# Kernel optimization log

Measured on AMD Instinct MI355X. Metric: run time of the kernel, lower is better.

Reference implementation:

```python
import jax, jax.numpy as jnp
import numpy as np

V, E, H, M = 32000, 512, 1024, 256
B, T, STRIDE = 2, 2048, 4


def setup_inputs() -> dict:
    key = jax.random.key(0)
    ks = jax.random.split(key, 18)
    s = 0.02
    n = jax.random.normal
    return {
        'input_ids': jax.random.randint(ks[0], (B, T), 0, V),
        'emb_weight': n(ks[1], (V, E)) * s,
        'gru_w_ih': n(ks[2], (3 * H, E)) * s,
        'gru_w_hh': n(ks[3], (3 * H, H)) * s,
        'gru_b_ih': n(ks[4], (3 * H,)) * s,
        'gru_b_hh': n(ks[5], (3 * H,)) * s,
        'q_w': n(ks[6], (M, H)) * s, 'q_b': n(ks[7], (M,)) * s,
        'k_w': n(ks[8], (M, H)) * s, 'k_b': n(ks[9], (M,)) * s,
        'hfc_w': n(ks[10], (4 * E, H)) * s, 'hfc_b': n(ks[11], (4 * E,)) * s,
        'hproj_w': n(ks[12], (E, 4 * E)) * s, 'hproj_b': n(ks[13], (E,)) * s,
        'v_w': n(ks[14], (E, E)) * s,
        'gate_w': n(ks[15], (E, H)) * s, 'gate_b': n(ks[16], (E,)) * s,
        'out_bias': jnp.zeros((V,), jnp.float32),
    }


def _gru(x, w_ih, w_hh, b_ih, b_hh):
    # x: [B,T,E] -> states [B,T,H]; single-layer torch GRU, h0 = 0
    h_dim = w_hh.shape[1]
    xg = jnp.einsum('bte,ge->btg', x, w_ih) + b_ih  # [B,T,3H] input gates precomputed

    def step(h, xg_t):
        gi_r, gi_z, gi_n = jnp.split(xg_t, 3, axis=-1)
        gh = h @ w_hh.T + b_hh
        gh_r, gh_z, gh_n = jnp.split(gh, 3, axis=-1)
        r = jax.nn.sigmoid(gi_r + gh_r)
        z = jax.nn.sigmoid(gi_z + gh_z)
        nstate = jnp.tanh(gi_n + r * gh_n)
        h_new = (1.0 - z) * nstate + z * h
        return h_new, h_new

    h0 = jnp.zeros((x.shape[0], h_dim), x.dtype)
    _, hs = jax.lax.scan(step, h0, jnp.swapaxes(xg, 0, 1))
    return jnp.swapaxes(hs, 0, 1)


def reference(input_ids, emb_weight, gru_w_ih, gru_w_hh, gru_b_ih, gru_b_hh,
              q_w, q_b, k_w, k_b, hfc_w, hfc_b, hproj_w, hproj_b,
              v_w, gate_w, gate_b, out_bias):
    emb = emb_weight[input_ids]                              # [B,T,E]
    states = _gru(emb, gru_w_ih, gru_w_hh, gru_b_ih, gru_b_hh)  # [B,T,H]; dropout is identity in eval

    head = jnp.square(jax.nn.relu(states @ hfc_w.T + hfc_b))  # [B,T,4E]
    base = head @ hproj_w.T + hproj_b                          # [B,T,E]

    # stride source pooling
    src_states = states[:, ::STRIDE]                         # [B,S,H]
    src_values = emb[:, ::STRIDE]                            # [B,S,E]
    seq_len = states.shape[1]
    src_pos = jnp.arange(0, seq_len, STRIDE)                 # [S]
    tgt_pos = jnp.arange(seq_len)                            # [T]
    mask = src_pos[None, :] < tgt_pos[:, None]               # [T,S] causal

    qk = states @ q_w.T + q_b                                # [B,T,M]
    mk = src_states @ k_w.T + k_b                            # [B,S,M]
    scores = jnp.einsum('btm,bsm->bts', qk, mk) / jnp.sqrt(jnp.array(M, qk.dtype))
    neg = jnp.finfo(scores.dtype).min
    scores = jnp.where(mask[None], scores, neg)
    att = jax.nn.softmax(scores, axis=-1)
    att = att * mask[None]
    att = att / jnp.maximum(att.sum(axis=-1, keepdims=True), 1e-6)

    retrieved = jnp.einsum('bts,bse->bte', att, src_values @ v_w.T)  # [B,T,E]
    mixed = base + jax.nn.sigmoid(states @ gate_w.T + gate_b) * retrieved
    return mixed @ emb_weight.T + out_bias                   # [B,T,V] tied logits
```

## Files before the change

### kernel.cpp

```cpp
#include <hip/hip_runtime.h>
#include <stdint.h>

typedef unsigned short u16;
typedef unsigned int u32;
typedef unsigned long long u64;
using f32x4 = __attribute__((ext_vector_type(4))) float;
using s16x8 = __attribute__((ext_vector_type(8))) short;
using s16x4 = __attribute__((ext_vector_type(4))) short;

#define DI __device__ __forceinline__

constexpr int kV = 32000, kE = 512, kH = 1024, kM = 256;
constexpr int kB = 2, kT = 2048, kS = 512;

DI u16 f2bf(float f) {
  u32 u = __float_as_uint(f);
  u32 r = (u + 0x7FFFu + ((u >> 16) & 1u)) >> 16;
  return (u16)r;
}
DI float bf2f(u16 u) { return __uint_as_float(((u32)u) << 16); }

DI void gload_lds16(const void* g, void* l) {
  __builtin_amdgcn_global_load_lds((const __attribute__((address_space(1))) void*)g,
                                   (__attribute__((address_space(3))) void*)l, 16, 0, 0);
}

__global__ __launch_bounds__(256)
void k_cvt(const float* __restrict__ in, u16* __restrict__ out, int n) {
  const int step = gridDim.x * blockDim.x;
  for (int i = blockIdx.x * blockDim.x + threadIdx.x; i * 4 < n; i += step) {
    f32x4 v = *(const f32x4*)(in + (size_t)i * 4);
    ushort4 o;
    o.x = f2bf(v[0]); o.y = f2bf(v[1]); o.z = f2bf(v[2]); o.w = f2bf(v[3]);
    *(ushort4*)(out + (size_t)i * 4) = o;
  }
}

__global__ __launch_bounds__(128)
void k_embed(const int* __restrict__ ids, const float* __restrict__ W,
             u16* __restrict__ out) {
  const int tok = blockIdx.x;
  const int id = ids[tok];
  f32x4 v = ((const f32x4*)(W + (size_t)id * kE))[threadIdx.x];
  ushort4 o;
  o.x = f2bf(v[0]); o.y = f2bf(v[1]); o.z = f2bf(v[2]); o.w = f2bf(v[3]);
  ((ushort4*)(out + (size_t)tok * kE))[threadIdx.x] = o;
}

__global__ __launch_bounds__(256)
void k_stride_copy(const u16* __restrict__ in, u16* __restrict__ out, int rowlen) {
  const int row = blockIdx.x;
  const int b = row / kS, s = row - b * kS;
  const u16* src = in + ((size_t)b * kT + 4 * s) * rowlen;
  u16* dst = out + (size_t)row * rowlen;
  for (int i = threadIdx.x; i < rowlen / 2; i += blockDim.x)
    reinterpret_cast<u32*>(dst)[i] = reinterpret_cast<const u32*>(src)[i];
}

template<int EPI>
__global__ __launch_bounds__(256)
void k_gemm(const u16* __restrict__ A, const u16* __restrict__ Bm,
            float* __restrict__ Cf, u16* __restrict__ Cb,
            const float* __restrict__ bias,
            int Mdim, int Ndim, int Kdim,
            long long sA, long long sB, long long sC,
            const float* __restrict__ addf, const float* __restrict__ mulf) {
  __shared__ __align__(16) u16 lA[128 * 32];
  __shared__ __align__(16) u16 lB[128 * 32];
  const int tid = threadIdx.x;
  const int bz = blockIdx.z;
  A += (long long)bz * sA;
  Bm += (long long)bz * sB;
  const long long coff = (long long)bz * sC;
  const int m0 = blockIdx.y * 128;
  const int n0 = blockIdx.x * 128;
  const int lane = tid & 63;
  const int wm = ((tid >> 6) >> 1) * 64;
  const int wn = ((tid >> 6) & 1) * 64;
  const int sr = tid >> 2;
  const int sc = (tid & 3) * 8;
  f32x4 acc[4][4] = {};
  for (int kt = 0; kt < Kdim; kt += 32) {
    gload_lds16(A + (long long)(m0 + sr) * Kdim + kt + sc,       &lA[tid * 8]);
    gload_lds16(A + (long long)(m0 + 64 + sr) * Kdim + kt + sc,  &lA[(tid + 256) * 8]);
    gload_lds16(Bm + (long long)(n0 + sr) * Kdim + kt + sc,      &lB[tid * 8]);
    gload_lds16(Bm + (long long)(n0 + 64 + sr) * Kdim + kt + sc, &lB[(tid + 256) * 8]);
    __syncthreads();
    s16x8 af[4], bfv[4];
    const int fro = lane & 15;
    const int fk = (lane >> 4) * 8;
#pragma unroll
    for (int f = 0; f < 4; f++) {
      af[f]  = *reinterpret_cast<const s16x8*>(&lA[(wm + f * 16 + fro) * 32 + fk]);
      bfv[f] = *reinterpret_cast<const s16x8*>(&lB[(wn + f * 16 + fro) * 32 + fk]);
    }
#pragma unroll
    for (int i = 0; i < 4; i++)
#pragma unroll
      for (int j = 0; j < 4; j++)
        acc[i][j] = __builtin_amdgcn_mfma_f32_16x16x32_bf16(af[i], bfv[j], acc[i][j], 0, 0, 0);
    __syncthreads();
  }
  const int crow = (lane >> 4) * 4;
  const int ccol = lane & 15;
#pragma unroll
  for (int i = 0; i < 4; i++) {
#pragma unroll
    for (int j = 0; j < 4; j++) {
      const int gn = n0 + wn + j * 16 + ccol;
      const float bs = bias ? bias[gn] : 0.0f;
#pragma unroll
      for (int r = 0; r < 4; r++) {
        const int gm = m0 + wm + i * 16 + crow + r;
        const long long off = coff + (long long)gm * Ndim + gn;
        float v = acc[i][j][r] + bs;
        if constexpr (EPI == 0) {
          Cf[off] = v;
        } else if constexpr (EPI == 1) {
          Cb[off] = f2bf(v);
        } else if constexpr (EPI == 2) {
          float uu = fmaxf(v, 0.0f);
          Cb[off] = f2bf(uu * uu);
        } else {
          float g = 1.0f / (1.0f + __expf(-v));
          Cb[off] = f2bf(addf[off] + g * mulf[off]);
        }
      }
    }
  }
}

__global__ __launch_bounds__(512, 1)
void k_gru(const float* __restrict__ xg, const u16* __restrict__ whh,
           const float* __restrict__ bhh, u64* __restrict__ hbuf,
           u32* __restrict__ flags, u16* __restrict__ states) {
  __shared__ __align__(16) u16 lw[48 * 1024];
  __shared__ __align__(16) float lh[1024];
  __shared__ u32 s_ticket, s_dec, s_res, s_bail;
  const int tid = threadIdx.x;
  u32 xcc;
  asm("s_getreg_b32 %0, hwreg(HW_REG_XCC_ID)" : "=s"(xcc));
  xcc &= 7u;
  if (tid == 0) {
    s_bail = 0u;
    u32 tk = atomicAdd(&flags[128 + xcc], 1u);
    if (tk == 31u) {
      u32 fidx = atomicAdd(&flags[136], 1u);
      if (fidx < 2u)
        __hip_atomic_store(&flags[140 + fidx], xcc + 1u, __ATOMIC_RELAXED, __HIP_MEMORY_SCOPE_AGENT);
    }
    s_ticket = tk;
    u32 d = 0;
    if (blockIdx.x == 0) {
      u32 polls = 0;
      for (;;) {
        if (__hip_atomic_load(&flags[136], __ATOMIC_RELAXED, __HIP_MEMORY_SCOPE_AGENT) >= 2u) {
          u32 a = __hip_atomic_load(&flags[140], __ATOMIC_RELAXED, __HIP_MEMORY_SCOPE_AGENT);
          u32 b = __hip_atomic_load(&flags[141], __ATOMIC_RELAXED, __HIP_MEMORY_SCOPE_AGENT);
          if (a && b) { d = 1u | ((a - 1u) << 8) | ((b - 1u) << 16); break; }
        }
        __builtin_amdgcn_s_sleep(1);
        if (++polls > 500000u) { d = 2u; break; }
      }
      __hip_atomic_store(&flags[137], d, __ATOMIC_RELAXED, __HIP_MEMORY_SCOPE_AGENT);
    } else {
      u32 polls = 0;
      while (!(d = __hip_atomic_load(&flags[137], __ATOMIC_RELAXED, __HIP_MEMORY_SCOPE_AGENT))) {
        __builtin_amdgcn_s_sleep(1);
        if (++polls > 1000000u) { d = 2u; break; }
      }
    }
    s_dec = d;
  }
  __syncthreads();
  const u32 dec = s_dec, ticket = s_ticket;
  int batch = -1;
  u32 slice = 0;
  bool l2m = false;
  if ((dec & 0xFFu) == 1u) {
    const u32 d0 = (dec >> 8) & 0xFFu, d1 = (dec >> 16) & 0xFFu;
    if (xcc == d0 && ticket < 32u) { batch = 0; slice = ticket; l2m = true; }
    else if (xcc == d1 && ticket < 32u) { batch = 1; slice = ticket; l2m = true; }
  } else {
    if (blockIdx.x < 64u) { batch = (int)(blockIdx.x >> 5); slice = blockIdx.x & 31u; }
  }
  if (batch < 0) return;

  if (l2m) {
    u32* hel = &flags[160 + batch * 32];
    u32* vot = &flags[224 + batch * 32];
    if (tid == 0) {
      u32 one = 1u;
      asm volatile("global_store_dword %0, %1, off" :: "v"(&hel[slice]), "v"(one) : "memory");
    }
    bool ok = true;
    if (tid < 32) {
      u32 v = 0, polls = 0;
      const u32* hp = &hel[tid];
      do {
        asm volatile("global_load_dword %0, %1, off nt\n\ts_waitcnt vmcnt(0)"
                     : "=v"(v) : "v"(hp) : "memory");
        if (v) break;
      } while (++polls < 200000u);
      ok = (v != 0);
    }
    u64 bad = __ballot(tid < 32 && !ok);
    if (tid == 0)
      __hip_atomic_store(&vot[slice], bad ? 2u : 1u, __ATOMIC_RELAXED, __HIP_MEMORY_SCOPE_AGENT);
    bool vb = false;
    if (tid < 32) {
      u32 v = 0, polls = 0;
      while (!(v = __hip_atomic_load(&vot[tid], __ATOMIC_RELAXED, __HIP_MEMORY_SCOPE_AGENT)))
        if (++polls > 1000000u) break;
      vb = (v != 1u);
    }
    u64 anybad = __ballot(tid < 32 && vb);
    if (tid == 0) s_res = (anybad == 0ull) ? 1u : 0u;
    __syncthreads();
    if (s_res == 0u) l2m = false;
  }

  const int j0 = (int)slice * 32;
  const int grp = tid >> 4;
  const int gl = tid & 15;
  const int j = j0 + grp;
  s16x4 wreg[3][16];
#pragma unroll
  for (int half = 0; half < 2; half++) {
#pragma unroll
    for (int r = 0; r < 12; r++) {
      int fi = tid + 512 * r;
      int lr = fi >> 7;
      int ce = (fi & 127) * 8;
      int lrow = half * 48 + lr;
      int gate = lrow >> 5, row = lrow & 31;
      gload_lds16(whh + ((size_t)gate * kH + j0 + row) * kH + ce, &lw[fi * 8]);
    }
    __syncthreads();
#pragma unroll
    for (int g = 0; g < 3; g++) {
      const int lrow = g * 32 + grp;
      if (lrow >= half * 48 && lrow < half * 48 + 48) {
        const u16* src = &lw[(size_t)(lrow - half * 48) * 1024];
#pragma unroll
        for (int i = 0; i < 16; i++)
          wreg[g][i] = *(const s16x4*)&src[4 * (gl + 16 * i)];
      }
    }
    __syncthreads();
  }

  const float bhr = bhh[j], bhz = bhh[kH + j], bhn = bhh[2 * kH + j];
  u32* fl = flags + batch * 64;
  const float* xgb = xg + (size_t)batch * kT * 3 * kH;
  u16* stb = states + (size_t)batch * kT * kH;
  float hkeep = 0.0f;
  float gi_r = 0.0f, gi_z = 0.0f, gi_n = 0.0f;
  if (gl == 0) { gi_r = xgb[j]; gi_z = xgb[kH + j]; gi_n = xgb[2 * kH + j]; }
  bool bailed = false;

  for (int t = 0; t < kT; t++) {
    u64* hc = hbuf + (size_t)(t & 1) * (kB * kH) + (size_t)batch * kH;
    u64* hn = hbuf + (size_t)((t + 1) & 1) * (kB * kH) + (size_t)batch * kH;
    const u32 want = (u32)t;
    if (!bailed) {
      u64 v0 = 0, v1 = 0;
      u32 polls = 0;
      if (l2m) {
        const u64* p0 = hc + tid;
        const u64* p1 = hc + tid + 512;
        for (;;) {
          asm volatile(
              "global_load_dwordx2 %0, %2, off nt\n\t"
              "global_load_dwordx2 %1, %3, off nt\n\t"
              "s_waitcnt vmcnt(0)"
              : "=&v"(v0), "=&v"(v1) : "v"(p0), "v"(p1) : "memory");
          if ((u32)(v0 >> 32) >= want && (u32)(v1 >> 32) >= want) break;
          if (++polls > 400000u) { bailed = true; break; }
        }
      } else {
        for (;;) {
          v0 = __hip_atomic_load(hc + tid, __ATOMIC_RELAXED, __HIP_MEMORY_SCOPE_AGENT);
          v1 = __hip_atomic_load(hc + tid + 512, __ATOMIC_RELAXED, __HIP_MEMORY_SCOPE_AGENT);
          if ((u32)(v0 >> 32) >= want && (u32)(v1 >> 32) >= want) break;
          if (++polls > 400000u) { bailed = true; break; }
        }
      }
      lh[tid] = __uint_as_float((u32)v0);
      lh[tid + 512] = __uint_as_float((u32)v1);
    }
    if (bailed) s_bail = 1u;
    __syncthreads();
    bailed = (s_bail != 0u);
    if (tid == 0) {
      u32 fv = (u32)(t + 1);
      if (l2m) asm volatile("global_store_dword %0, %1, off" :: "v"(&fl[slice]), "v"(fv) : "memory");
      else __hip_atomic_store(&fl[slice], fv, __ATOMIC_RELAXED, __HIP_MEMORY_SCOPE_AGENT);
    }
    u32 myf = 0;
    if (tid < 32 && !bailed) {
      if (l2m) asm volatile("global_load_dword %0, %1, off nt\n\ts_waitcnt vmcnt(0)"
                            : "=v"(myf) : "v"(&fl[tid]) : "memory");
      else myf = __hip_atomic_load(&fl[tid], __ATOMIC_RELAXED, __HIP_MEMORY_SCOPE_AGENT);
    }
    float ar = 0.f, az = 0.f, an = 0.f;
#pragma unroll
    for (int i = 0; i < 16; i++) {
      f32x4 h4 = *(const f32x4*)&lh[4 * (gl + 16 * i)];
      s16x4 w0 = wreg[0][i], w1 = wreg[1][i], w2 = wreg[2][i];
#pragma unroll
      for (int e = 0; e < 4; e++) {
        ar += bf2f((u16)w0[e]) * h4[e];
        az += bf2f((u16)w1[e]) * h4[e];
        an += bf2f((u16)w2[e]) * h4[e];
      }
    }
#pragma unroll
    for (int m = 8; m >= 1; m >>= 1) {
      ar += __shfl_xor(ar, m, 16);
      az += __shfl_xor(az, m, 16);
      an += __shfl_xor(an, m, 16);
    }
    if (!bailed) {
      u32 polls = 0;
      while (__ballot(tid < 32 && myf < want) != 0ull) {
        if (++polls > 400000u) { bailed = true; break; }
        if (tid < 32) {
          if (l2m) asm volatile("global_load_dword %0, %1, off nt\n\ts_waitcnt vmcnt(0)"
                                : "=v"(myf) : "v"(&fl[tid]) : "memory");
          else myf = __hip_atomic_load(&fl[tid], __ATOMIC_RELAXED, __HIP_MEMORY_SCOPE_AGENT);
        }
      }
    }
    __syncthreads();
    if (gl == 0) {
      float r = 1.0f / (1.0f + __expf(-(gi_r + ar + bhr)));
      float z = 1.0f / (1.0f + __expf(-(gi_z + az + bhz)));
      float n = tanhf(gi_n + r * (an + bhn));
      float hnew = (1.0f - z) * n + z * hkeep;
      hkeep = hnew;
      u64 pk = ((u64)(u32)(t + 1) << 32) | (u64)__float_as_uint(hnew);
      if (l2m) asm volatile("global_store_dwordx2 %0, %1, off" :: "v"(hn + j), "v"(pk) : "memory");
      else __hip_atomic_store(hn + j, pk, __ATOMIC_RELAXED, __HIP_MEMORY_SCOPE_AGENT);
      stb[(size_t)t * kH + j] = f2bf(hnew);
      if (t + 1 < kT) {
        const float* xp = xgb + (size_t)(t + 1) * 3 * kH;
        gi_r = xp[j]; gi_z = xp[kH + j]; gi_n = xp[2 * kH + j];
      }
    }
  }
}

__global__ __launch_bounds__(256)
void k_softmax(const float* __restrict__ sc, u16* __restrict__ att) {
  const int row = blockIdx.x * 4 + (threadIdx.x >> 6);
  const int lane = threadIdx.x & 63;
  const int t = row & (kT - 1);
  const int nv = (t + 3) >> 2;
  const float* src = sc + (long long)row * kS;
  u16* dst = att + (long long)row * kS;
  f32x4 v0 = *(const f32x4*)(src + lane * 8);
  f32x4 v1 = *(const f32x4*)(src + lane * 8 + 4);
  float x[8];
  float mx = -3.0e38f;
#pragma unroll
  for (int e = 0; e < 8; e++) {
    float val = ((e < 4) ? v0[e & 3] : v1[e & 3]) * 0.0625f;
    x[e] = val;
    if (lane * 8 + e < nv) mx = fmaxf(mx, val);
  }
#pragma unroll
  for (int m = 32; m >= 1; m >>= 1) mx = fmaxf(mx, __shfl_xor(mx, m, 64));
  float p[8];
  float sum = 0.0f;
#pragma unroll
  for (int e = 0; e < 8; e++) {
    p[e] = (lane * 8 + e < nv) ? __expf(x[e] - mx) : 0.0f;
    sum += p[e];
  }
#pragma unroll
  for (int m = 32; m >= 1; m >>= 1) sum += __shfl_xor(sum, m, 64);
  const float inv = (nv == 0) ? 0.0f : (1.0f / sum);
  ushort4 o0, o1;
  o0.x = f2bf(p[0] * inv); o0.y = f2bf(p[1] * inv);
  o0.z = f2bf(p[2] * inv); o0.w = f2bf(p[3] * inv);
  o1.x = f2bf(p[4] * inv); o1.y = f2bf(p[5] * inv);
  o1.z = f2bf(p[6] * inv); o1.w = f2bf(p[7] * inv);
  *(ushort4*)(dst + lane * 8) = o0;
  *(ushort4*)(dst + lane * 8 + 4) = o1;
}

static void gemm(int epi, const u16* A, const u16* Bm, float* Cf, u16* Cb,
                 const float* bias, int M, int N, int K, int batch,
                 long long sA, long long sB, long long sC,
                 const float* addf, const float* mulf, hipStream_t st) {
  dim3 g((unsigned)(N / 128), (unsigned)(M / 128), (unsigned)batch), b(256);
  switch (epi) {
    case 0: k_gemm<0><<<g, b, 0, st>>>(A, Bm, Cf, Cb, bias, M, N, K, sA, sB, sC, addf, mulf); break;
    case 1: k_gemm<1><<<g, b, 0, st>>>(A, Bm, Cf, Cb, bias, M, N, K, sA, sB, sC, addf, mulf); break;
    case 2: k_gemm<2><<<g, b, 0, st>>>(A, Bm, Cf, Cb, bias, M, N, K, sA, sB, sC, addf, mulf); break;
    default: k_gemm<3><<<g, b, 0, st>>>(A, Bm, Cf, Cb, bias, M, N, K, sA, sB, sC, addf, mulf); break;
  }
}

extern "C" void kernel_launch(void* const* d_in, const int* in_sizes, int n_in,
                              void* d_out, int out_size, void* d_ws, size_t ws_size,
                              hipStream_t stream) {
  (void)in_sizes; (void)n_in; (void)out_size;
  const int* ids      = (const int*)d_in[0];
  const float* embW   = (const float*)d_in[1];
  const float* w_ih   = (const float*)d_in[2];
  const float* w_hh   = (const float*)d_in[3];
  const float* b_ih   = (const float*)d_in[4];
  const float* b_hh   = (const float*)d_in[5];
  const float* q_w    = (const float*)d_in[6];
  const float* q_b    = (const float*)d_in[7];
  const float* k_w    = (const float*)d_in[8];
  const float* k_b    = (const float*)d_in[9];
  const float* hfc_w  = (const float*)d_in[10];
  const float* hfc_b  = (const float*)d_in[11];
  const float* hproj_w  = (const float*)d_in[12];
  const float* hproj_b  = (const float*)d_in[13];
  const float* v_w    = (const float*)d_in[14];
  const float* gate_w = (const float*)d_in[15];
  const float* gate_b = (const float*)d_in[16];
  const float* out_b  = (const float*)d_in[17];
  float* out = (float*)d_out;

  char* ws = (char*)d_ws;
  size_t off = 0;
  auto alloc = [&](size_t bytes) -> void* {
    void* p = ws + off;
    off += (bytes + 255) & ~(size_t)255;
    return p;
  };
  u16* embw_bf   = (u16*)alloc((size_t)kV * kE * 2);
  u16* states_bf = (u16*)alloc((size_t)kB * kT * kH * 2);
  u16* emb_bf    = (u16*)alloc((size_t)kB * kT * kE * 2);
  u16* qw_bf     = (u16*)alloc((size_t)kM * kH * 2);
  u16* kw_bf     = (u16*)alloc((size_t)kM * kH * 2);
  u16* hfcw_bf   = (u16*)alloc((size_t)4 * kE * kH * 2);
  u16* hprojw_bf = (u16*)alloc((size_t)kE * 4 * kE * 2);
  u16* vw_bf     = (u16*)alloc((size_t)kE * kE * 2);
  u16* gatew_bf  = (u16*)alloc((size_t)kE * kH * 2);
  u64* hbuf      = (u64*)alloc((size_t)2 * kB * kH * 8);
  u32* flags     = (u32*)alloc(2048);
  const size_t s0 = off;
  u16* wih_bf    = (u16*)alloc((size_t)3 * kH * kE * 2);
  u16* whh_bf    = (u16*)alloc((size_t)3 * kH * kH * 2);
  float* xg      = (float*)alloc((size_t)kB * kT * 3 * kH * 4);
  const size_t endG = off;
  off = s0;
  u16* head_bf   = (u16*)alloc((size_t)kB * kT * 4 * kE * 2);
  float* basef   = (float*)alloc((size_t)kB * kT * kE * 4);
  u16* qk_bf     = (u16*)alloc((size_t)kB * kT * kM * 2);
  u16* srcs_bf   = (u16*)alloc((size_t)kB * kS * kH * 2);
  u16* srcv_bf   = (u16*)alloc((size_t)kB * kS * kE * 2);
  u16* mk_bf     = (u16*)alloc((size_t)kB * kS * kM * 2);
  float* scoresf = (float*)alloc((size_t)kB * kT * kS * 4);
  u16* att_bf    = (u16*)alloc((size_t)kB * kT * kS * 2);
  u16* svt_bf    = (u16*)alloc((size_t)kB * kE * kS * 2);
  float* retrf   = (float*)alloc((size_t)kB * kT * kE * 4);
  u16* mixed_bf  = (u16*)alloc((size_t)kB * kT * kE * 2);
  const size_t endA = off;
  const size_t need = (endG > endA ? endG : endA);
  if (ws_size < need) return;

  dim3 b256(256);
  k_cvt<<<1024, b256, 0, stream>>>(w_ih, wih_bf, 3 * kH * kE);
  k_cvt<<<1024, b256, 0, stream>>>(w_hh, whh_bf, 3 * kH * kH);
  k_cvt<<<1024, b256, 0, stream>>>(q_w, qw_bf, kM * kH);
  k_cvt<<<1024, b256, 0, stream>>>(k_w, kw_bf, kM * kH);
  k_cvt<<<1024, b256, 0, stream>>>(hfc_w, hfcw_bf, 4 * kE * kH);
  k_cvt<<<1024, b256, 0, stream>>>(hproj_w, hprojw_bf, kE * 4 * kE);
  k_cvt<<<1024, b256, 0, stream>>>(v_w, vw_bf, kE * kE);
  k_cvt<<<1024, b256, 0, stream>>>(gate_w, gatew_bf, kE * kH);
  k_cvt<<<2048, b256, 0, stream>>>(embW, embw_bf, kV * kE);
  k_embed<<<kB * kT, 128, 0, stream>>>(ids, embW, emb_bf);

  gemm(0, emb_bf, wih_bf, xg, nullptr, b_ih, kB * kT, 3 * kH, kE,
       1, 0, 0, 0, nullptr, nullptr, stream);

  hipMemsetAsync(hbuf, 0, (size_t)2 * kB * kH * 8 + 2048, stream);
  k_gru<<<256, dim3(512), 0, stream>>>(xg, whh_bf, b_hh, hbuf, flags, states_bf);

  gemm(2, states_bf, hfcw_bf, nullptr, head_bf, hfc_b, kB * kT, 4 * kE, kH,
       1, 0, 0, 0, nullptr, nullptr, stream);
  gemm(0, head_bf, hprojw_bf, basef, nullptr, hproj_b, kB * kT, kE, 4 * kE,
       1, 0, 0, 0, nullptr, nullptr, stream);
  gemm(1, states_bf, qw_bf, nullptr, qk_bf, q_b, kB * kT, kM, kH,
       1, 0, 0, 0, nullptr, nullptr, stream);
  k_stride_copy<<<kB * kS, b256, 0, stream>>>(states_bf, srcs_bf, kH);
  k_stride_copy<<<kB * kS, b256, 0, stream>>>(emb_bf, srcv_bf, kE);
  gemm(1, srcs_bf, kw_bf, nullptr, mk_bf, k_b, kB * kS, kM, kH,
       1, 0, 0, 0, nullptr, nullptr, stream);
  gemm(0, qk_bf, mk_bf, scoresf, nullptr, nullptr, kT, kS, kM, kB,
       (long long)kT * kM, (long long)kS * kM, (long long)kT * kS,
       nullptr, nullptr, stream);
  k_softmax<<<(kB * kT) / 4, b256, 0, stream>>>(scoresf, att_bf);
  gemm(1, vw_bf, srcv_bf, nullptr, svt_bf, nullptr, kE, kS, kE, kB,
       0, (long long)kS * kE, (long long)kE * kS, nullptr, nullptr, stream);
  gemm(0, att_bf, svt_bf, retrf, nullptr, nullptr, kT, kE, kS, kB,
       (long long)kT * kS, (long long)kE * kS, (long long)kT * kE,
       nullptr, nullptr, stream);
  gemm(3, states_bf, gatew_bf, nullptr, mixed_bf, gate_b, kB * kT, kE, kH,
       1, 0, 0, 0, basef, retrf, stream);
  gemm(0, mixed_bf, embw_bf, out, nullptr, out_b, kB * kT, kV, kE,
       1, 0, 0, 0, nullptr, nullptr, stream);
}
```

Measured before the change: 4.429 ms.

## Double-buffer GRU hidden state, drop per-step barrier, preconvert weights to fp32

The GRU recurrent kernel now double-buffers the shared hidden-state vector, so the trailing __syncthreads at the end of each timestep can be removed. Every wave polls the peer flags itself instead of only the first 32 threads. The bf16 recurrent weights are converted to fp32 once into registers, which removes the per-step conversion from the dot product. tanh is replaced by an exp-based formula, and wall-clock watchdog timeouts are added to the spin loops. The fp32 weights double register use, and __launch_bounds__ min-blocks changes from 1 to 2, which risks spills. The exp-based tanh can overflow to inf/inf = NaN for large arguments.

```diff
diff --git a/kernel.cpp b/kernel.cpp
--- a/kernel.cpp
+++ b/kernel.cpp
@@ -12,6 +12,7 @@
 
 constexpr int kV = 32000, kE = 512, kH = 1024, kM = 256;
 constexpr int kB = 2, kT = 2048, kS = 512;
+constexpr u64 kWatchdogTicks = 200000000ull;
 
 DI u16 f2bf(float f) {
   u32 u = __float_as_uint(f);
@@ -23,6 +24,9 @@
 DI void gload_lds16(const void* g, void* l) {
   __builtin_amdgcn_global_load_lds((const __attribute__((address_space(1))) void*)g,
                                    (__attribute__((address_space(3))) void*)l, 16, 0, 0);
+}
+DI bool wd_expired(u64 t0) {
+  return (__builtin_amdgcn_s_memrealtime() - t0) > kWatchdogTicks;
 }
 
 __global__ __launch_bounds__(256)
@@ -130,14 +134,15 @@
   }
 }
 
-__global__ __launch_bounds__(512, 1)
+__global__ __launch_bounds__(512, 2)
 void k_gru(const float* __restrict__ xg, const u16* __restrict__ whh,
            const float* __restrict__ bhh, u64* __restrict__ hbuf,
            u32* __restrict__ flags, u16* __restrict__ states) {
   __shared__ __align__(16) u16 lw[48 * 1024];
-  __shared__ __align__(16) float lh[1024];
+  __shared__ __align__(16) float lh[2][1024];
   __shared__ u32 s_ticket, s_dec, s_res, s_bail;
   const int tid = threadIdx.x;
+  const u64 wd0 = __builtin_amdgcn_s_memrealtime();
   u32 xcc;
   asm("s_getreg_b32 %0, hwreg(HW_REG_XCC_ID)" : "=s"(xcc));
   xcc &= 7u;
@@ -160,14 +165,14 @@
           if (a && b) { d = 1u | ((a - 1u) << 8) | ((b - 1u) << 16); break; }
         }
         __builtin_amdgcn_s_sleep(1);
-        if (++polls > 500000u) { d = 2u; break; }
+        if (++polls > 500000u || wd_expired(wd0)) { d = 2u; break; }
       }
       __hip_atomic_store(&flags[137], d, __ATOMIC_RELAXED, __HIP_MEMORY_SCOPE_AGENT);
     } else {
       u32 polls = 0;
       while (!(d = __hip_atomic_load(&flags[137], __ATOMIC_RELAXED, __HIP_MEMORY_SCOPE_AGENT))) {
         __builtin_amdgcn_s_sleep(1);
-        if (++polls > 1000000u) { d = 2u; break; }
+        if (++polls > 1000000u || wd_expired(wd0)) { d = 2u; break; }
       }
     }
     s_dec = d;
@@ -201,6 +206,7 @@
         asm volatile("global_load_dword %0, %1, off nt\n\ts_waitcnt vmcnt(0)"
                      : "=v"(v) : "v"(hp) : "memory");
         if (v) break;
+        if (wd_expired(wd0)) break;
       } while (++polls < 200000u);
       ok = (v != 0);
     }
@@ -211,7 +217,7 @@
     if (tid < 32) {
       u32 v = 0, polls = 0;
       while (!(v = __hip_atomic_load(&vot[tid], __ATOMIC_RELAXED, __HIP_MEMORY_SCOPE_AGENT)))
-        if (++polls > 1000000u) break;
+        if (++polls > 1000000u || wd_expired(wd0)) break;
       vb = (v != 1u);
     }
     u64 anybad = __ballot(tid < 32 && vb);
@@ -224,7 +230,7 @@
   const int grp = tid >> 4;
   const int gl = tid & 15;
   const int j = j0 + grp;
-  s16x4 wreg[3][16];
+  f32x4 wreg[3][16];
 #pragma unroll
   for (int half = 0; half < 2; half++) {
 #pragma unroll
@@ -243,8 +249,13 @@
       if (lrow >= half * 48 && lrow < half * 48 + 48) {
         const u16* src = &lw[(size_t)(lrow - half * 48) * 1024];
 #pragma unroll
-        for (int i = 0; i < 16; i++)
-          wreg[g][i] = *(const s16x4*)&src[4 * (gl + 16 * i)];
+        for (int i = 0; i < 16; i++) {
+          s16x4 w = *(const s16x4*)&src[4 * (gl + 16 * i)];
+          f32x4 wf;
+          wf[0] = bf2f((u16)w[0]); wf[1] = bf2f((u16)w[1]);
+          wf[2] = bf2f((u16)w[2]); wf[3] = bf2f((u16)w[3]);
+          wreg[g][i] = wf;
+        }
       }
     }
     __syncthreads();
@@ -252,6 +263,7 @@
 
   const float bhr = bhh[j], bhz = bhh[kH + j], bhn = bhh[2 * kH + j];
   u32* fl = flags + batch * 64;
+  const int fli = tid & 31;
   const float* xgb = xg + (size_t)batch * kT * 3 * kH;
   u16* stb = states + (size_t)batch * kT * kH;
   float hkeep = 0.0f;
@@ -263,6 +275,7 @@
     u64* hc = hbuf + (size_t)(t & 1) * (kB * kH) + (size_t)batch * kH;
     u64* hn = hbuf + (size_t)((t + 1) & 1) * (kB * kH) + (size_t)batch * kH;
     const u32 want = (u32)t;
+    float* lhb = lh[t & 1];
     if (!bailed) {
       u64 v0 = 0, v1 = 0;
       u32 polls = 0;
@@ -277,6 +290,7 @@
               : "=&v"(v0), "=&v"(v1) : "v"(p0), "v"(p1) : "memory");
           if ((u32)(v0 >> 32) >= want && (u32)(v1 >> 32) >= want) break;
           if (++polls > 400000u) { bailed = true; break; }
+          if (!(polls & 4095u) && wd_expired(wd0)) { bailed = true; break; }
         }
       } else {
         for (;;) {
@@ -284,10 +298,11 @@
           v1 = __hip_atomic_load(hc + tid + 512, __ATOMIC_RELAXED, __HIP_MEMORY_SCOPE_AGENT);
           if ((u32)(v0 >> 32) >= want && (u32)(v1 >> 32) >= want) break;
           if (++polls > 400000u) { bailed = true; break; }
+          if (!(polls & 4095u) && wd_expired(wd0)) { bailed = true; break; }
         }
       }
-      lh[tid] = __uint_as_float((u32)v0);
-      lh[tid + 512] = __uint_as_float((u32)v1);
+      lhb[tid] = __uint_as_float((u32)v0);
+      lhb[tid + 512] = __uint_as_float((u32)v1);
     }
     if (bailed) s_bail = 1u;
     __syncthreads();
@@ -298,21 +313,21 @@
       else __hip_atomic_store(&fl[slice], fv, __ATOMIC_RELAXED, __HIP_MEMORY_SCOPE_AGENT);
     }
     u32 myf = 0;
-    if (tid < 32 && !bailed) {
+    if (!bailed) {
       if (l2m) asm volatile("global_load_dword %0, %1, off nt\n\ts_waitcnt vmcnt(0)"
-                            : "=v"(myf) : "v"(&fl[tid]) : "memory");
-      else myf = __hip_atomic_load(&fl[tid], __ATOMIC_RELAXED, __HIP_MEMORY_SCOPE_AGENT);
+                            : "=v"(myf) : "v"(&fl[fli]) : "memory");
+      else myf = __hip_atomic_load(&fl[fli], __ATOMIC_RELAXED, __HIP_MEMORY_SCOPE_AGENT);
     }
     float ar = 0.f, az = 0.f, an = 0.f;
 #pragma unroll
     for (int i = 0; i < 16; i++) {
-      f32x4 h4 = *(const f32x4*)&lh[4 * (gl + 16 * i)];
-      s16x4 w0 = wreg[0][i], w1 = wreg[1][i], w2 = wreg[2][i];
+      f32x4 h4 = *(const f32x4*)&lhb[4 * (gl + 16 * i)];
+      f32x4 w0 = wreg[0][i], w1 = wreg[1][i], w2 = wreg[2][i];
 #pragma unroll
       for (int e = 0; e < 4; e++) {
-        ar += bf2f((u16)w0[e]) * h4[e];
-        az += bf2f((u16)w1[e]) * h4[e];
-        an += bf2f((u16)w2[e]) * h4[e];
+        ar += w0[e] * h4[e];
+        az += w1[e] * h4[e];
+        an += w2[e] * h4[e];
       }
     }
 #pragma unroll
@@ -323,20 +338,19 @@
     }
     if (!bailed) {
       u32 polls = 0;
-      while (__ballot(tid < 32 && myf < want) != 0ull) {
+      while (__ballot(myf < want) != 0ull) {
         if (++polls > 400000u) { bailed = true; break; }
-        if (tid < 32) {
-          if (l2m) asm volatile("global_load_dword %0, %1, off nt\n\ts_waitcnt vmcnt(0)"
-                                : "=v"(myf) : "v"(&fl[tid]) : "memory");
-          else myf = __hip_atomic_load(&fl[tid], __ATOMIC_RELAXED, __HIP_MEMORY_SCOPE_AGENT);
-        }
-      }
-    }
-    __syncthreads();
+        if (!(polls & 4095u) && wd_expired(wd0)) { bailed = true; break; }
+        if (l2m) asm volatile("global_load_dword %0, %1, off nt\n\ts_waitcnt vmcnt(0)"
+                              : "=v"(myf) : "v"(&fl[fli]) : "memory");
+        else myf = __hip_atomic_load(&fl[fli], __ATOMIC_RELAXED, __HIP_MEMORY_SCOPE_AGENT);
+      }
+    }
     if (gl == 0) {
       float r = 1.0f / (1.0f + __expf(-(gi_r + ar + bhr)));
       float z = 1.0f / (1.0f + __expf(-(gi_z + az + bhz)));
-      float n = tanhf(gi_n + r * (an + bhn));
+      float ex = __expf(2.0f * (gi_n + r * (an + bhn)));
+      float n = (ex - 1.0f) / (ex + 1.0f);
       float hnew = (1.0f - z) * n + z * hkeep;
       hkeep = hnew;
       u64 pk = ((u64)(u32)(t + 1) << 32) | (u64)__float_as_uint(hnew);
```

New measurement: 4.102 ms (median of 2 runs). 1.08x faster.
